# Performance work log

Hardware: AMD Instinct MI355X
Metric: run time of the kernel (lower is better)

Reference implementation:

```python
import jax, jax.numpy as jnp
import numpy as np

N = 100000      # nodes
DEG = 16        # uniform in-degree
E = N * DEG     # edges
D = 2           # pseudo-coordinate dim
K = 4           # gaussian kernels
IN_F = 128      # input feature dim
OUT_F = 32      # output feature dim


def setup_inputs() -> dict:
    key = jax.random.key(0)
    ks = jax.random.split(key, 6)
    # dst-major CSR: node i owns edges rowptr[i]:rowptr[i+1]
    rowptr = (jnp.arange(N + 1) * DEG).astype(jnp.int32)
    colind = jax.random.randint(ks[0], (E,), 0, N, dtype=jnp.int32)  # src ids
    # CSC mirror (consumed by fused kernel's backward only; not used in fwd math)
    colptr = rowptr
    rowind = colind
    permute = jnp.arange(E, dtype=jnp.int32)  # CSR edge order -> pseudo order
    feat = jax.random.normal(ks[1], (N, IN_F), jnp.float32)
    pseudo = jax.random.normal(ks[2], (E, D), jnp.float32)
    # parameters (per reset_parameters: xavier fc, mu~N(0,0.1), inv_sigma=1, bias=0)
    gain = 1.4142135  # relu gain
    std = gain * (2.0 / (IN_F + K * OUT_F)) ** 0.5
    fc_w = jax.random.normal(ks[3], (K * OUT_F, IN_F), jnp.float32) * std
    mu = jax.random.normal(ks[4], (K, D), jnp.float32) * 0.1
    inv_sigma = jnp.ones((K, D), jnp.float32)
    bias = jnp.zeros((OUT_F,), jnp.float32)
    return {"rowptr": rowptr, "colind": colind, "colptr": colptr,
            "rowind": rowind, "permute": permute, "feat": feat,
            "pseudo": pseudo, "fc_w": fc_w, "mu": mu,
            "inv_sigma": inv_sigma, "bias": bias}


def reference(rowptr, colind, colptr, rowind, permute, feat, pseudo,
              fc_w, mu, inv_sigma, bias):
    n = feat.shape[0]
    e = colind.shape[0]
    k, d = mu.shape
    out_f = bias.shape[0]
    # fc(feat).view(-1, K, OUT)
    node_feat = (feat @ fc_w.T).reshape(n, k, out_f)  # [N,K,F]
    # per-edge gaussian kernel weights from pseudo coords (CSR edge order)
    pe = pseudo[permute]                               # [E,D]
    diff = (pe[:, None, :] - mu[None, :, :]) * inv_sigma[None, :, :]  # [E,K,D]
    w = jnp.exp(-0.5 * jnp.sum(diff * diff, axis=-1))  # [E,K]
    # gather src kernel-features, weight, sum over kernels (.sum(1) commutes)
    msg = jnp.einsum('ek,ekf->ef', w, node_feat[colind])  # [E,F]
    # scatter-sum into dst nodes
    deg = rowptr[1:] - rowptr[:-1]
    dst = jnp.repeat(jnp.arange(n, dtype=jnp.int32), deg, total_repeat_length=e)
    rst = jax.ops.segment_sum(msg, dst, num_segments=n)  # [N,F]
    return rst + bias
```

## Files before the change

### kernel.cpp

```cpp
#include <hip/hip_runtime.h>

#define NN     100000
#define DEG    16
#define IN_F   128
#define OUT_F  32
#define KK     4
#define JDIM   (KK * OUT_F)
#define TRS    70

typedef __attribute__((ext_vector_type(8))) short short8;
typedef __attribute__((ext_vector_type(4))) short short4v;
typedef __attribute__((ext_vector_type(4))) float floatx4;

static __device__ __forceinline__ unsigned short f2bf(float f) {
  unsigned int u = __builtin_bit_cast(unsigned int, f);
  u += 0x7fffu + ((u >> 16) & 1u);
  return (unsigned short)(u >> 16);
}

__global__ __launch_bounds__(256) void gmm_cvt_w(
    const float* __restrict__ fc_w, unsigned short* __restrict__ wcvt)
{
  const int g = blockIdx.x * 256 + threadIdx.x;
  const int c = g & 15, q = (g >> 4) & 3, t = (g >> 6) & 7, s = g >> 9;
  const float* src = fc_w + (size_t)(t * 16 + c) * IN_F + s * 32 + q * 8;
  const float4 f0 = *(const float4*)src;
  const float4 f1 = *(const float4*)(src + 4);
  short8 v;
  v[0] = (short)f2bf(f0.x); v[1] = (short)f2bf(f0.y);
  v[2] = (short)f2bf(f0.z); v[3] = (short)f2bf(f0.w);
  v[4] = (short)f2bf(f1.x); v[5] = (short)f2bf(f1.y);
  v[6] = (short)f2bf(f1.z); v[7] = (short)f2bf(f1.w);
  *(short8*)(wcvt + (size_t)g * 8) = v;
}

__global__ __launch_bounds__(256) void gmm_fc_mfma(
    const float* __restrict__ feat, const unsigned short* __restrict__ wcvt,
    unsigned short* __restrict__ nf)
{
  __shared__ uint4 s_wfrag[2048];
  __shared__ unsigned short s_tr[4][32 * TRS];

  const int tid  = threadIdx.x;
  const int lane = tid & 63;
  const int wv   = tid >> 6;

  const uint4* wsrc = (const uint4*)wcvt;
#pragma unroll
  for (int r = 0; r < 8; ++r)
    s_wfrag[tid + r * 256] = wsrc[tid + r * 256];
  __syncthreads();

  const int tile = blockIdx.x * 4 + wv;
  if (tile * 32 >= NN) return;
  const int m0 = tile * 32;
  const int c  = lane & 15;
  const int q  = lane >> 4;

  const float* frow0 = feat + (size_t)(m0 + c) * IN_F + q * 8;
  const float* frow1 = frow0 + (size_t)16 * IN_F;
  float4 fr[2][4][2];
#pragma unroll
  for (int s = 0; s < 4; ++s) {
    fr[0][s][0] = *(const float4*)(frow0 + s * 32);
    fr[0][s][1] = *(const float4*)(frow0 + s * 32 + 4);
    fr[1][s][0] = *(const float4*)(frow1 + s * 32);
    fr[1][s][1] = *(const float4*)(frow1 + s * 32 + 4);
  }

  short8 bv[2][4];
#pragma unroll
  for (int g = 0; g < 2; ++g) {
#pragma unroll
    for (int s = 0; s < 4; ++s) {
      const float4 b0 = fr[g][s][0];
      const float4 b1 = fr[g][s][1];
      short8 v;
      v[0] = (short)f2bf(b0.x); v[1] = (short)f2bf(b0.y);
      v[2] = (short)f2bf(b0.z); v[3] = (short)f2bf(b0.w);
      v[4] = (short)f2bf(b1.x); v[5] = (short)f2bf(b1.y);
      v[6] = (short)f2bf(b1.z); v[7] = (short)f2bf(b1.w);
      bv[g][s] = v;
    }
  }

  floatx4 acc[2][8];
#pragma unroll
  for (int g = 0; g < 2; ++g)
#pragma unroll
    for (int t = 0; t < 8; ++t) acc[g][t] = (floatx4){0.f, 0.f, 0.f, 0.f};

  const short8* wlds = (const short8*)s_wfrag;
#pragma unroll
  for (int s = 0; s < 4; ++s) {
#pragma unroll
    for (int t = 0; t < 8; ++t) {
      const short8 av = wlds[(s * 8 + t) * 64 + lane];
      acc[0][t] = __builtin_amdgcn_mfma_f32_16x16x32_bf16(av, bv[0][s], acc[0][t], 0, 0, 0);
      acc[1][t] = __builtin_amdgcn_mfma_f32_16x16x32_bf16(av, bv[1][s], acc[1][t], 0, 0, 0);
    }
  }

  unsigned short* tr = &s_tr[wv][0];
#pragma unroll
  for (int th = 0; th < 2; ++th) {
#pragma unroll
    for (int g = 0; g < 2; ++g) {
#pragma unroll
      for (int tt = 0; tt < 4; ++tt) {
        const int t = th * 4 + tt;
        short4v p;
        p[0] = (short)f2bf(acc[g][t][0]); p[1] = (short)f2bf(acc[g][t][1]);
        p[2] = (short)f2bf(acc[g][t][2]); p[3] = (short)f2bf(acc[g][t][3]);
        *(short4v*)&tr[(g * 16 + c) * TRS + tt * 16 + q * 4] = p;
      }
    }
#pragma unroll
    for (int jj = 0; jj < 4; ++jj) {
      const int chunk = jj * 64 + lane;
      const int row = chunk >> 3;
      const int co  = chunk & 7;
      const uint4 v = *(const uint4*)&tr[row * TRS + co * 8];
      *(uint4*)(nf + (size_t)(m0 + row) * JDIM + th * 64 + co * 8) = v;
    }
  }
}

__global__ __launch_bounds__(256) void gmm_edge_gather(
    const int* __restrict__ rowptr, const int* __restrict__ colind,
    const int* __restrict__ permute, const float* __restrict__ pseudo,
    const float* __restrict__ mu, const float* __restrict__ inv_sigma,
    const float* __restrict__ bias, const unsigned short* __restrict__ nf,
    float* __restrict__ out)
{
  __shared__ int   s_src[1024];
  __shared__ float s_w[1024][4];

  const int tid    = threadIdx.x;
  const int node0  = blockIdx.x * 64;
  const int nvalid = (NN - node0 < 64) ? (NN - node0) : 64;

  float mx[KK], my[KK], sx[KK], sy[KK];
#pragma unroll
  for (int k = 0; k < KK; ++k) {
    mx[k] = mu[k * 2 + 0];
    my[k] = mu[k * 2 + 1];
    sx[k] = inv_sigma[k * 2 + 0];
    sy[k] = inv_sigma[k * 2 + 1];
  }

#pragma unroll
  for (int r = 0; r < 4; ++r) {
    const int t  = tid + r * 256;
    const int nl = t >> 4;
    if (nl < nvalid) {
      const int e   = rowptr[node0 + nl] + (t & 15);
      const int pe  = permute[e];
      s_src[t] = colind[e];
      const float px = pseudo[(size_t)pe * 2 + 0];
      const float py = pseudo[(size_t)pe * 2 + 1];
#pragma unroll
      for (int k = 0; k < KK; ++k) {
        const float dx = (px - mx[k]) * sx[k];
        const float dy = (py - my[k]) * sy[k];
        s_w[t][k] = __expf(-0.5f * (dx * dx + dy * dy));
      }
    }
  }
  __syncthreads();

  const int nl = tid >> 2;
  const int f8 = tid & 3;
  if (nl >= nvalid) return;

  float acc[8];
  {
    const float4 b0 = *(const float4*)&bias[f8 * 8];
    const float4 b1 = *(const float4*)&bias[f8 * 8 + 4];
    acc[0] = b0.x; acc[1] = b0.y; acc[2] = b0.z; acc[3] = b0.w;
    acc[4] = b1.x; acc[5] = b1.y; acc[6] = b1.z; acc[7] = b1.w;
  }

  const int tbase = nl * 16;
#pragma unroll
  for (int i = 0; i < DEG; ++i) {
    const int e = (i + nl) & 15;
    const int t = tbase + e;
    const int src = s_src[t];
    const float4 w4 = *(const float4*)&s_w[t][0];
    const float wv[4] = {w4.x, w4.y, w4.z, w4.w};
    const unsigned short* row = nf + (size_t)src * JDIM + f8 * 8;
#pragma unroll
    for (int k = 0; k < KK; ++k) {
      const uint4 v = *(const uint4*)(row + k * 32);
      const float wk = wv[k];
      acc[0] += wk * __uint_as_float(v.x << 16);
      acc[1] += wk * __uint_as_float(v.x & 0xffff0000u);
      acc[2] += wk * __uint_as_float(v.y << 16);
      acc[3] += wk * __uint_as_float(v.y & 0xffff0000u);
      acc[4] += wk * __uint_as_float(v.z << 16);
      acc[5] += wk * __uint_as_float(v.z & 0xffff0000u);
      acc[6] += wk * __uint_as_float(v.w << 16);
      acc[7] += wk * __uint_as_float(v.w & 0xffff0000u);
    }
  }

  float4 o0 = {acc[0], acc[1], acc[2], acc[3]};
  float4 o1 = {acc[4], acc[5], acc[6], acc[7]};
  float* op = out + (size_t)(node0 + nl) * OUT_F + f8 * 8;
  *(float4*)(op)     = o0;
  *(float4*)(op + 4) = o1;
}

extern "C" void kernel_launch(void* const* d_in, const int* in_sizes, int n_in,
                              void* d_out, int out_size, void* d_ws, size_t ws_size,
                              hipStream_t stream) {
  const int*   rowptr    = (const int*)d_in[0];
  const int*   colind    = (const int*)d_in[1];
  const int*   permute   = (const int*)d_in[4];
  const float* feat      = (const float*)d_in[5];
  const float* pseudo    = (const float*)d_in[6];
  const float* fc_w      = (const float*)d_in[7];
  const float* mu        = (const float*)d_in[8];
  const float* inv_sigma = (const float*)d_in[9];
  const float* bias      = (const float*)d_in[10];
  float* out = (float*)d_out;

  unsigned short* nf   = (unsigned short*)d_ws;
  unsigned short* wcvt = (unsigned short*)((char*)d_ws + (26u << 20));

  gmm_cvt_w<<<8, 256, 0, stream>>>(fc_w, wcvt);
  gmm_fc_mfma<<<(NN / 32 + 3) / 4, 256, 0, stream>>>(feat, wcvt, nf);
  gmm_edge_gather<<<(NN + 63) / 64, 256, 0, stream>>>(
      rowptr, colind, permute, pseudo, mu, inv_sigma, bias, nf, out);
}
```

Baseline: 193.2 us.

## Fuse weight conversion, FC MFMA and edge gather into one persistent kernel

The three launches are merged into one persistent kernel with 512 blocks. Each block converts the fc weights to bf16 straight into LDS, then grid-strides over the FC tiles. A software grid barrier (an atomic counter reset by a memset) separates the FC phase from the grid-strided edge-gather phase. This removes the launch gaps and the global weight-scratch round trip, but adds barrier spinning, redundant per-block weight conversion, and a deadlock risk if not all 512 blocks are co-resident.

```diff
diff --git a/kernel.cpp b/kernel.cpp
--- a/kernel.cpp
+++ b/kernel.cpp
@@ -7,6 +7,9 @@
 #define KK     4
 #define JDIM   (KK * OUT_F)
 #define TRS    70
+#define GRIDB  512
+#define NTILES ((NN + 31) / 32)
+#define NGRP   ((NN + 63) / 64)
 
 typedef __attribute__((ext_vector_type(8))) short short8;
 typedef __attribute__((ext_vector_type(4))) short short4v;
@@ -18,127 +21,127 @@
   return (unsigned short)(u >> 16);
 }
 
-__global__ __launch_bounds__(256) void gmm_cvt_w(
-    const float* __restrict__ fc_w, unsigned short* __restrict__ wcvt)
+__global__ __launch_bounds__(256, 2) void gmm_fused(
+    const int* __restrict__ rowptr, const int* __restrict__ colind,
+    const int* __restrict__ permute, const float* __restrict__ feat,
+    const float* __restrict__ pseudo, const float* __restrict__ fc_w,
+    const float* __restrict__ mu, const float* __restrict__ inv_sigma,
+    const float* __restrict__ bias, unsigned short* __restrict__ nf,
+    unsigned int* __restrict__ barrier_ctr, float* __restrict__ out)
 {
-  const int g = blockIdx.x * 256 + threadIdx.x;
-  const int c = g & 15, q = (g >> 4) & 3, t = (g >> 6) & 7, s = g >> 9;
-  const float* src = fc_w + (size_t)(t * 16 + c) * IN_F + s * 32 + q * 8;
-  const float4 f0 = *(const float4*)src;
-  const float4 f1 = *(const float4*)(src + 4);
-  short8 v;
-  v[0] = (short)f2bf(f0.x); v[1] = (short)f2bf(f0.y);
-  v[2] = (short)f2bf(f0.z); v[3] = (short)f2bf(f0.w);
-  v[4] = (short)f2bf(f1.x); v[5] = (short)f2bf(f1.y);
-  v[6] = (short)f2bf(f1.z); v[7] = (short)f2bf(f1.w);
-  *(short8*)(wcvt + (size_t)g * 8) = v;
-}
-
-__global__ __launch_bounds__(256) void gmm_fc_mfma(
-    const float* __restrict__ feat, const unsigned short* __restrict__ wcvt,
-    unsigned short* __restrict__ nf)
-{
-  __shared__ uint4 s_wfrag[2048];
-  __shared__ unsigned short s_tr[4][32 * TRS];
+  __shared__ __align__(16) char smem[50688];
+  uint4* s_wfrag = (uint4*)smem;
+  unsigned short* s_tr_base = (unsigned short*)(smem + 32768);
 
   const int tid  = threadIdx.x;
   const int lane = tid & 63;
   const int wv   = tid >> 6;
 
-  const uint4* wsrc = (const uint4*)wcvt;
-#pragma unroll
-  for (int r = 0; r < 8; ++r)
-    s_wfrag[tid + r * 256] = wsrc[tid + r * 256];
+#pragma unroll
+  for (int r = 0; r < 8; ++r) {
+    const int g = r * 256 + tid;
+    const int c = g & 15, q = (g >> 4) & 3, t = (g >> 6) & 7, s = g >> 9;
+    const float* src = fc_w + (size_t)(t * 16 + c) * IN_F + s * 32 + q * 8;
+    const float4 f0 = *(const float4*)src;
+    const float4 f1 = *(const float4*)(src + 4);
+    short8 v;
+    v[0] = (short)f2bf(f0.x); v[1] = (short)f2bf(f0.y);
+    v[2] = (short)f2bf(f0.z); v[3] = (short)f2bf(f0.w);
+    v[4] = (short)f2bf(f1.x); v[5] = (short)f2bf(f1.y);
+    v[6] = (short)f2bf(f1.z); v[7] = (short)f2bf(f1.w);
+    *(short8*)(s_wfrag + g) = v;
+  }
   __syncthreads();
 
-  const int tile = blockIdx.x * 4 + wv;
-  if (tile * 32 >= NN) return;
-  const int m0 = tile * 32;
-  const int c  = lane & 15;
-  const int q  = lane >> 4;
-
-  const float* frow0 = feat + (size_t)(m0 + c) * IN_F + q * 8;
-  const float* frow1 = frow0 + (size_t)16 * IN_F;
-  float4 fr[2][4][2];
-#pragma unroll
-  for (int s = 0; s < 4; ++s) {
-    fr[0][s][0] = *(const float4*)(frow0 + s * 32);
-    fr[0][s][1] = *(const float4*)(frow0 + s * 32 + 4);
-    fr[1][s][0] = *(const float4*)(frow1 + s * 32);
-    fr[1][s][1] = *(const float4*)(frow1 + s * 32 + 4);
-  }
-
-  short8 bv[2][4];
-#pragma unroll
-  for (int g = 0; g < 2; ++g) {
+  const short8* wlds = (const short8*)s_wfrag;
+  unsigned short* tr = s_tr_base + wv * (32 * TRS);
+
+  for (int tile = blockIdx.x * 4 + wv; tile < NTILES; tile += GRIDB * 4) {
+    const int m0 = tile * 32;
+    const int c  = lane & 15;
+    const int q  = lane >> 4;
+
+    const float* frow0 = feat + (size_t)(m0 + c) * IN_F + q * 8;
+    const float* frow1 = frow0 + (size_t)16 * IN_F;
+    float4 fr[2][4][2];
 #pragma unroll
     for (int s = 0; s < 4; ++s) {
-      const float4 b0 = fr[g][s][0];
-      const float4 b1 = fr[g][s][1];
-      short8 v;
-      v[0] = (short)f2bf(b0.x); v[1] = (short)f2bf(b0.y);
-      v[2] = (short)f2bf(b0.z); v[3] = (short)f2bf(b0.w);
-      v[4] = (short)f2bf(b1.x); v[5] = (short)f2bf(b1.y);
-      v[6] = (short)f2bf(b1.z); v[7] = (short)f2bf(b1.w);
-      bv[g][s] = v;
-    }
-  }
-
-  floatx4 acc[2][8];
-#pragma unroll
-  for (int g = 0; g < 2; ++g)
-#pragma unroll
-    for (int t = 0; t < 8; ++t) acc[g][t] = (floatx4){0.f, 0.f, 0.f, 0.f};
-
-  const short8* wlds = (const short8*)s_wfrag;
-#pragma unroll
-  for (int s = 0; s < 4; ++s) {
-#pragma unroll
-    for (int t = 0; t < 8; ++t) {
-      const short8 av = wlds[(s * 8 + t) * 64 + lane];
-      acc[0][t] = __builtin_amdgcn_mfma_f32_16x16x32_bf16(av, bv[0][s], acc[0][t], 0, 0, 0);
-      acc[1][t] = __builtin_amdgcn_mfma_f32_16x16x32_bf16(av, bv[1][s], acc[1][t], 0, 0, 0);
-    }
-  }
-
-  unsigned short* tr = &s_tr[wv][0];
-#pragma unroll
-  for (int th = 0; th < 2; ++th) {
+      fr[0][s][0] = *(const float4*)(frow0 + s * 32);
+      fr[0][s][1] = *(const float4*)(frow0 + s * 32 + 4);
+      fr[1][s][0] = *(const float4*)(frow1 + s * 32);
+      fr[1][s][1] = *(const float4*)(frow1 + s * 32 + 4);
+    }
+
+    short8 bv[2][4];
 #pragma unroll
     for (int g = 0; g < 2; ++g) {
 #pragma unroll
-      for (int tt = 0; tt < 4; ++tt) {
-        const int t = th * 4 + tt;
-        short4v p;
-        p[0] = (short)f2bf(acc[g][t][0]); p[1] = (short)f2bf(acc[g][t][1]);
-        p[2] = (short)f2bf(acc[g][t][2]); p[3] = (short)f2bf(acc[g][t][3]);
-        *(short4v*)&tr[(g * 16 + c) * TRS + tt * 16 + q * 4] = p;
-      }
-    }
-#pragma unroll
-    for (int jj = 0; jj < 4; ++jj) {
-      const int chunk = jj * 64 + lane;
-      const int row = chunk >> 3;
-      const int co  = chunk & 7;
-      const uint4 v = *(const uint4*)&tr[row * TRS + co * 8];
-      *(uint4*)(nf + (size_t)(m0 + row) * JDIM + th * 64 + co * 8) = v;
-    }
-  }
-}
-
-__global__ __launch_bounds__(256) void gmm_edge_gather(
-    const int* __restrict__ rowptr, const int* __restrict__ colind,
-    const int* __restrict__ permute, const float* __restrict__ pseudo,
-    const float* __restrict__ mu, const float* __restrict__ inv_sigma,
-    const float* __restrict__ bias, const unsigned short* __restrict__ nf,
-    float* __restrict__ out)
-{
-  __shared__ int   s_src[1024];
-  __shared__ float s_w[1024][4];
-
-  const int tid    = threadIdx.x;
-  const int node0  = blockIdx.x * 64;
-  const int nvalid = (NN - node0 < 64) ? (NN - node0) : 64;
+      for (int s = 0; s < 4; ++s) {
+        const float4 b0 = fr[g][s][0];
+        const float4 b1 = fr[g][s][1];
+        short8 v;
+        v[0] = (short)f2bf(b0.x); v[1] = (short)f2bf(b0.y);
+        v[2] = (short)f2bf(b0.z); v[3] = (short)f2bf(b0.w);
+        v[4] = (short)f2bf(b1.x); v[5] = (short)f2bf(b1.y);
+        v[6] = (short)f2bf(b1.z); v[7] = (short)f2bf(b1.w);
+        bv[g][s] = v;
+      }
+    }
+
+    floatx4 acc[2][8];
+#pragma unroll
+    for (int g = 0; g < 2; ++g)
+#pragma unroll
+      for (int t = 0; t < 8; ++t) acc[g][t] = (floatx4){0.f, 0.f, 0.f, 0.f};
+
+#pragma unroll
+    for (int s = 0; s < 4; ++s) {
+#pragma unroll
+      for (int t = 0; t < 8; ++t) {
+        const short8 av = wlds[(s * 8 + t) * 64 + lane];
+        acc[0][t] = __builtin_amdgcn_mfma_f32_16x16x32_bf16(av, bv[0][s], acc[0][t], 0, 0, 0);
+        acc[1][t] = __builtin_amdgcn_mfma_f32_16x16x32_bf16(av, bv[1][s], acc[1][t], 0, 0, 0);
+      }
+    }
+
+#pragma unroll
+    for (int th = 0; th < 2; ++th) {
+#pragma unroll
+      for (int g = 0; g < 2; ++g) {
+#pragma unroll
+        for (int tt = 0; tt < 4; ++tt) {
+          const int t = th * 4 + tt;
+          short4v p;
+          p[0] = (short)f2bf(acc[g][t][0]); p[1] = (short)f2bf(acc[g][t][1]);
+          p[2] = (short)f2bf(acc[g][t][2]); p[3] = (short)f2bf(acc[g][t][3]);
+          *(short4v*)&tr[(g * 16 + c) * TRS + tt * 16 + q * 4] = p;
+        }
+      }
+#pragma unroll
+      for (int jj = 0; jj < 4; ++jj) {
+        const int chunk = jj * 64 + lane;
+        const int row = chunk >> 3;
+        const int co  = chunk & 7;
+        const uint4 v = *(const uint4*)&tr[row * TRS + co * 8];
+        *(uint4*)(nf + (size_t)(m0 + row) * JDIM + th * 64 + co * 8) = v;
+      }
+    }
+  }
+
+  __threadfence();
+  __syncthreads();
+  if (tid == 0) {
+    __hip_atomic_fetch_add(barrier_ctr, 1u, __ATOMIC_RELEASE,
+                           __HIP_MEMORY_SCOPE_AGENT);
+    while (__hip_atomic_load(barrier_ctr, __ATOMIC_ACQUIRE,
+                             __HIP_MEMORY_SCOPE_AGENT) < (unsigned)GRIDB)
+      __builtin_amdgcn_s_sleep(8);
+  }
+  __syncthreads();
+  __threadfence();
+
+  int*  s_src = (int*)smem;
+  float (*s_wB)[4] = (float(*)[4])(smem + 4096);
 
   float mx[KK], my[KK], sx[KK], sy[KK];
 #pragma unroll
@@ -149,67 +152,74 @@
     sy[k] = inv_sigma[k * 2 + 1];
   }
 
-#pragma unroll
-  for (int r = 0; r < 4; ++r) {
-    const int t  = tid + r * 256;
-    const int nl = t >> 4;
-    if (nl < nvalid) {
-      const int e   = rowptr[node0 + nl] + (t & 15);
-      const int pe  = permute[e];
-      s_src[t] = colind[e];
-      const float px = pseudo[(size_t)pe * 2 + 0];
-      const float py = pseudo[(size_t)pe * 2 + 1];
-#pragma unroll
-      for (int k = 0; k < KK; ++k) {
-        const float dx = (px - mx[k]) * sx[k];
-        const float dy = (py - my[k]) * sy[k];
-        s_w[t][k] = __expf(-0.5f * (dx * dx + dy * dy));
-      }
-    }
-  }
-  __syncthreads();
-
   const int nl = tid >> 2;
   const int f8 = tid & 3;
-  if (nl >= nvalid) return;
-
-  float acc[8];
-  {
-    const float4 b0 = *(const float4*)&bias[f8 * 8];
-    const float4 b1 = *(const float4*)&bias[f8 * 8 + 4];
-    acc[0] = b0.x; acc[1] = b0.y; acc[2] = b0.z; acc[3] = b0.w;
-    acc[4] = b1.x; acc[5] = b1.y; acc[6] = b1.z; acc[7] = b1.w;
-  }
-
-  const int tbase = nl * 16;
-#pragma unroll
-  for (int i = 0; i < DEG; ++i) {
-    const int e = (i + nl) & 15;
-    const int t = tbase + e;
-    const int src = s_src[t];
-    const float4 w4 = *(const float4*)&s_w[t][0];
-    const float wv[4] = {w4.x, w4.y, w4.z, w4.w};
-    const unsigned short* row = nf + (size_t)src * JDIM + f8 * 8;
-#pragma unroll
-    for (int k = 0; k < KK; ++k) {
-      const uint4 v = *(const uint4*)(row + k * 32);
-      const float wk = wv[k];
-      acc[0] += wk * __uint_as_float(v.x << 16);
-      acc[1] += wk * __uint_as_float(v.x & 0xffff0000u);
-      acc[2] += wk * __uint_as_float(v.y << 16);
-      acc[3] += wk * __uint_as_float(v.y & 0xffff0000u);
-      acc[4] += wk * __uint_as_float(v.z << 16);
-      acc[5] += wk * __uint_as_float(v.z & 0xffff0000u);
-      acc[6] += wk * __uint_as_float(v.w << 16);
-      acc[7] += wk * __uint_as_float(v.w & 0xffff0000u);
-    }
-  }
-
-  float4 o0 = {acc[0], acc[1], acc[2], acc[3]};
-  float4 o1 = {acc[4], acc[5], acc[6], acc[7]};
-  float* op = out + (size_t)(node0 + nl) * OUT_F + f8 * 8;
-  *(float4*)(op)     = o0;
-  *(float4*)(op + 4) = o1;
+
+  for (int grp = blockIdx.x; grp < NGRP; grp += GRIDB) {
+    __syncthreads();
+    const int node0  = grp * 64;
+    const int nvalid = (NN - node0 < 64) ? (NN - node0) : 64;
+
+#pragma unroll
+    for (int r = 0; r < 4; ++r) {
+      const int t  = tid + r * 256;
+      const int nle = t >> 4;
+      if (nle < nvalid) {
+        const int e   = rowptr[node0 + nle] + (t & 15);
+        const int pe  = permute[e];
+        s_src[t] = colind[e];
+        const float px = pseudo[(size_t)pe * 2 + 0];
+        const float py = pseudo[(size_t)pe * 2 + 1];
+#pragma unroll
+        for (int k = 0; k < KK; ++k) {
+          const float dx = (px - mx[k]) * sx[k];
+          const float dy = (py - my[k]) * sy[k];
+          s_wB[t][k] = __expf(-0.5f * (dx * dx + dy * dy));
+        }
+      }
+    }
+    __syncthreads();
+
+    if (nl < nvalid) {
+      float acc[8];
+      {
+        const float4 b0 = *(const float4*)&bias[f8 * 8];
+        const float4 b1 = *(const float4*)&bias[f8 * 8 + 4];
+        acc[0] = b0.x; acc[1] = b0.y; acc[2] = b0.z; acc[3] = b0.w;
+        acc[4] = b1.x; acc[5] = b1.y; acc[6] = b1.z; acc[7] = b1.w;
+      }
+
+      const int tbase = nl * 16;
+#pragma unroll
+      for (int i = 0; i < DEG; ++i) {
+        const int e = (i + nl) & 15;
+        const int t = tbase + e;
+        const int src = s_src[t];
+        const float4 w4 = *(const float4*)&s_wB[t][0];
+        const float wvv[4] = {w4.x, w4.y, w4.z, w4.w};
+        const unsigned short* row = nf + (size_t)src * JDIM + f8 * 8;
+#pragma unroll
+        for (int k = 0; k < KK; ++k) {
+          const uint4 v = *(const uint4*)(row + k * 32);
+          const float wk = wvv[k];
+          acc[0] += wk * __uint_as_float(v.x << 16);
+          acc[1] += wk * __uint_as_float(v.x & 0xffff0000u);
+          acc[2] += wk * __uint_as_float(v.y << 16);
+          acc[3] += wk * __uint_as_float(v.y & 0xffff0000u);
+          acc[4] += wk * __uint_as_float(v.z << 16);
+          acc[5] += wk * __uint_as_float(v.z & 0xffff0000u);
+          acc[6] += wk * __uint_as_float(v.w << 16);
+          acc[7] += wk * __uint_as_float(v.w & 0xffff0000u);
+        }
+      }
+
+      float4 o0 = {acc[0], acc[1], acc[2], acc[3]};
+      float4 o1 = {acc[4], acc[5], acc[6], acc[7]};
+      float* op = out + (size_t)(node0 + nl) * OUT_F + f8 * 8;
+      *(float4*)(op)     = o0;
+      *(float4*)(op + 4) = o1;
+    }
+  }
 }
 
 extern "C" void kernel_launch(void* const* d_in, const int* in_sizes, int n_in,
@@ -226,11 +236,12 @@
   const float* bias      = (const float*)d_in[10];
   float* out = (float*)d_out;
 
-  unsigned short* nf   = (unsigned short*)d_ws;
-  unsigned short* wcvt = (unsigned short*)((char*)d_ws + (26u << 20));
-
-  gmm_cvt_w<<<8, 256, 0, stream>>>(fc_w, wcvt);
-  gmm_fc_mfma<<<(NN / 32 + 3) / 4, 256, 0, stream>>>(feat, wcvt, nf);
-  gmm_edge_gather<<<(NN + 63) / 64, 256, 0, stream>>>(
-      rowptr, colind, permute, pseudo, mu, inv_sigma, bias, nf, out);
+  unsigned short* nf = (unsigned short*)d_ws;
+  unsigned int* barrier_ctr = (unsigned int*)((char*)d_ws + (26u << 20));
+
+  hipMemsetAsync(barrier_ctr, 0, sizeof(unsigned int), stream);
+
+  gmm_fused<<<GRIDB, 256, 0, stream>>>(
+      rowptr, colind, permute, feat, pseudo, fc_w, mu, inv_sigma,
+      bias, nf, barrier_ctr, out);
 }
```

Measured after the change: 353.8 us. +83.1%, slower.

## Fuse weight conversion into FC kernel and use wave-per-node edge gather

Applied to the files above, without the earlier changes.

The separate fc_w-to-bf16 conversion kernel is removed. Each FC block now converts the weight fragments itself while filling shared memory, which saves a launch and a workspace round trip but repeats the conversion in every block. The edge gather is rewritten as a grid-stride loop where one wavefront handles one node. Its 64 lanes each cover a 16-byte slice of a source row for four edges at a time and compute the Gaussian weight inline, then sum over kernels and edges with xor shuffles. This drops the LDS staging and the block-level barrier, at the cost of 32 shuffles per node and fewer independent loads in flight per lane.

```diff
diff --git a/kernel.cpp b/kernel.cpp
--- a/kernel.cpp
+++ b/kernel.cpp
@@ -7,6 +7,7 @@
 #define KK     4
 #define JDIM   (KK * OUT_F)
 #define TRS    70
+#define NTILES ((NN + 31) / 32)
 
 typedef __attribute__((ext_vector_type(8))) short short8;
 typedef __attribute__((ext_vector_type(4))) short short4v;
@@ -18,24 +19,8 @@
   return (unsigned short)(u >> 16);
 }
 
-__global__ __launch_bounds__(256) void gmm_cvt_w(
-    const float* __restrict__ fc_w, unsigned short* __restrict__ wcvt)
-{
-  const int g = blockIdx.x * 256 + threadIdx.x;
-  const int c = g & 15, q = (g >> 4) & 3, t = (g >> 6) & 7, s = g >> 9;
-  const float* src = fc_w + (size_t)(t * 16 + c) * IN_F + s * 32 + q * 8;
-  const float4 f0 = *(const float4*)src;
-  const float4 f1 = *(const float4*)(src + 4);
-  short8 v;
-  v[0] = (short)f2bf(f0.x); v[1] = (short)f2bf(f0.y);
-  v[2] = (short)f2bf(f0.z); v[3] = (short)f2bf(f0.w);
-  v[4] = (short)f2bf(f1.x); v[5] = (short)f2bf(f1.y);
-  v[6] = (short)f2bf(f1.z); v[7] = (short)f2bf(f1.w);
-  *(short8*)(wcvt + (size_t)g * 8) = v;
-}
-
 __global__ __launch_bounds__(256) void gmm_fc_mfma(
-    const float* __restrict__ feat, const unsigned short* __restrict__ wcvt,
+    const float* __restrict__ feat, const float* __restrict__ fc_w,
     unsigned short* __restrict__ nf)
 {
   __shared__ uint4 s_wfrag[2048];
@@ -45,10 +30,20 @@
   const int lane = tid & 63;
   const int wv   = tid >> 6;
 
-  const uint4* wsrc = (const uint4*)wcvt;
-#pragma unroll
-  for (int r = 0; r < 8; ++r)
-    s_wfrag[tid + r * 256] = wsrc[tid + r * 256];
+#pragma unroll
+  for (int r = 0; r < 8; ++r) {
+    const int g = r * 256 + tid;
+    const int c = g & 15, q = (g >> 4) & 3, t = (g >> 6) & 7, s = g >> 9;
+    const float* src = fc_w + (size_t)(t * 16 + c) * IN_F + s * 32 + q * 8;
+    const float4 f0 = *(const float4*)src;
+    const float4 f1 = *(const float4*)(src + 4);
+    short8 v;
+    v[0] = (short)f2bf(f0.x); v[1] = (short)f2bf(f0.y);
+    v[2] = (short)f2bf(f0.z); v[3] = (short)f2bf(f0.w);
+    v[4] = (short)f2bf(f1.x); v[5] = (short)f2bf(f1.y);
+    v[6] = (short)f2bf(f1.z); v[7] = (short)f2bf(f1.w);
+    *(short8*)&s_wfrag[g] = v;
+  }
   __syncthreads();
 
   const int tile = blockIdx.x * 4 + wv;
@@ -133,83 +128,65 @@
     const float* __restrict__ bias, const unsigned short* __restrict__ nf,
     float* __restrict__ out)
 {
-  __shared__ int   s_src[1024];
-  __shared__ float s_w[1024][4];
-
-  const int tid    = threadIdx.x;
-  const int node0  = blockIdx.x * 64;
-  const int nvalid = (NN - node0 < 64) ? (NN - node0) : 64;
-
-  float mx[KK], my[KK], sx[KK], sy[KK];
-#pragma unroll
-  for (int k = 0; k < KK; ++k) {
-    mx[k] = mu[k * 2 + 0];
-    my[k] = mu[k * 2 + 1];
-    sx[k] = inv_sigma[k * 2 + 0];
-    sy[k] = inv_sigma[k * 2 + 1];
-  }
-
-#pragma unroll
-  for (int r = 0; r < 4; ++r) {
-    const int t  = tid + r * 256;
-    const int nl = t >> 4;
-    if (nl < nvalid) {
-      const int e   = rowptr[node0 + nl] + (t & 15);
-      const int pe  = permute[e];
-      s_src[t] = colind[e];
-      const float px = pseudo[(size_t)pe * 2 + 0];
-      const float py = pseudo[(size_t)pe * 2 + 1];
-#pragma unroll
-      for (int k = 0; k < KK; ++k) {
-        const float dx = (px - mx[k]) * sx[k];
-        const float dy = (py - my[k]) * sy[k];
-        s_w[t][k] = __expf(-0.5f * (dx * dx + dy * dy));
-      }
-    }
-  }
-  __syncthreads();
-
-  const int nl = tid >> 2;
-  const int f8 = tid & 3;
-  if (nl >= nvalid) return;
-
-  float acc[8];
-  {
-    const float4 b0 = *(const float4*)&bias[f8 * 8];
-    const float4 b1 = *(const float4*)&bias[f8 * 8 + 4];
-    acc[0] = b0.x; acc[1] = b0.y; acc[2] = b0.z; acc[3] = b0.w;
-    acc[4] = b1.x; acc[5] = b1.y; acc[6] = b1.z; acc[7] = b1.w;
-  }
-
-  const int tbase = nl * 16;
-#pragma unroll
-  for (int i = 0; i < DEG; ++i) {
-    const int e = (i + nl) & 15;
-    const int t = tbase + e;
-    const int src = s_src[t];
-    const float4 w4 = *(const float4*)&s_w[t][0];
-    const float wv[4] = {w4.x, w4.y, w4.z, w4.w};
-    const unsigned short* row = nf + (size_t)src * JDIM + f8 * 8;
-#pragma unroll
-    for (int k = 0; k < KK; ++k) {
-      const uint4 v = *(const uint4*)(row + k * 32);
-      const float wk = wv[k];
-      acc[0] += wk * __uint_as_float(v.x << 16);
-      acc[1] += wk * __uint_as_float(v.x & 0xffff0000u);
-      acc[2] += wk * __uint_as_float(v.y << 16);
-      acc[3] += wk * __uint_as_float(v.y & 0xffff0000u);
-      acc[4] += wk * __uint_as_float(v.z << 16);
-      acc[5] += wk * __uint_as_float(v.z & 0xffff0000u);
-      acc[6] += wk * __uint_as_float(v.w << 16);
-      acc[7] += wk * __uint_as_float(v.w & 0xffff0000u);
-    }
-  }
-
-  float4 o0 = {acc[0], acc[1], acc[2], acc[3]};
-  float4 o1 = {acc[4], acc[5], acc[6], acc[7]};
-  float* op = out + (size_t)(node0 + nl) * OUT_F + f8 * 8;
-  *(float4*)(op)     = o0;
-  *(float4*)(op + 4) = o1;
+  const int tid  = threadIdx.x;
+  const int lane = tid & 63;
+  const int gw   = blockIdx.x * 4 + (tid >> 6);
+  const int NW   = gridDim.x * 4;
+
+  const int es = lane >> 4;
+  const int j  = lane & 15;
+  const int k  = (lane >> 2) & 3;
+  const int m  = lane & 3;
+  const int h  = (lane >> 2) & 1;
+
+  const float mxk = mu[k * 2 + 0];
+  const float myk = mu[k * 2 + 1];
+  const float sxk = inv_sigma[k * 2 + 0];
+  const float syk = inv_sigma[k * 2 + 1];
+  const float4 b4 = *(const float4*)&bias[m * 8 + h * 4];
+
+  for (int n = gw; n < NN; n += NW) {
+    const int eb = rowptr[n];
+    float acc[8];
+#pragma unroll
+    for (int t = 0; t < 8; ++t) acc[t] = 0.f;
+
+#pragma unroll
+    for (int p = 0; p < 4; ++p) {
+      const int e  = eb + p * 4 + es;
+      const int pe = permute[e];
+      const int src = colind[e];
+      const float2 pp = *(const float2*)&pseudo[(size_t)pe * 2];
+      const float dx = (pp.x - mxk) * sxk;
+      const float dy = (pp.y - myk) * syk;
+      const float w  = __expf(-0.5f * (dx * dx + dy * dy));
+      const uint4 v = *(const uint4*)(nf + (size_t)src * JDIM + j * 8);
+      acc[0] += w * __uint_as_float(v.x << 16);
+      acc[1] += w * __uint_as_float(v.x & 0xffff0000u);
+      acc[2] += w * __uint_as_float(v.y << 16);
+      acc[3] += w * __uint_as_float(v.y & 0xffff0000u);
+      acc[4] += w * __uint_as_float(v.z << 16);
+      acc[5] += w * __uint_as_float(v.z & 0xffff0000u);
+      acc[6] += w * __uint_as_float(v.w << 16);
+      acc[7] += w * __uint_as_float(v.w & 0xffff0000u);
+    }
+
+#pragma unroll
+    for (int mask = 4; mask <= 32; mask <<= 1) {
+#pragma unroll
+      for (int t = 0; t < 8; ++t)
+        acc[t] += __shfl_xor(acc[t], mask, 64);
+    }
+
+    if (lane < 8) {
+      float4 o;
+      o.x = acc[h * 4 + 0] + b4.x;
+      o.y = acc[h * 4 + 1] + b4.y;
+      o.z = acc[h * 4 + 2] + b4.z;
+      o.w = acc[h * 4 + 3] + b4.w;
+      *(float4*)(out + (size_t)n * OUT_F + m * 8 + h * 4) = o;
+    }
+  }
 }
 
 extern "C" void kernel_launch(void* const* d_in, const int* in_sizes, int n_in,
@@ -226,11 +203,9 @@
   const float* bias      = (const float*)d_in[10];
   float* out = (float*)d_out;
 
-  unsigned short* nf   = (unsigned short*)d_ws;
-  unsigned short* wcvt = (unsigned short*)((char*)d_ws + (26u << 20));
-
-  gmm_cvt_w<<<8, 256, 0, stream>>>(fc_w, wcvt);
-  gmm_fc_mfma<<<(NN / 32 + 3) / 4, 256, 0, stream>>>(feat, wcvt, nf);
-  gmm_edge_gather<<<(NN + 63) / 64, 256, 0, stream>>>(
+  unsigned short* nf = (unsigned short*)d_ws;
+
+  gmm_fc_mfma<<<(NN / 32 + 3) / 4, 256, 0, stream>>>(feat, fc_w, nf);
+  gmm_edge_gather<<<2048, 256, 0, stream>>>(
       rowptr, colind, permute, pseudo, mu, inv_sigma, bias, nf, out);
 }
```

Result: slower. 203.1 us (+5.1%).
